# Kernel optimization log

Hardware: AMD Instinct MI355X
Metric: run time of the kernel (lower is better)

## Reference

```python
import jax, jax.numpy as jnp
import numpy as np

N_A, N_P = 50000, 100000          # author / paper node counts
E_W, E_C = 1600000, 3200000       # writes & written_by edges, cites edges
NEG_SLOPE = 0.2                   # DGL GATConv default leaky_relu slope
EPS = 1e-12                       # F.normalize eps


def _gat(h_src, h_dst, src, dst, W, al, ar, b, n_dst):
    """DGL GATConv: fc -> per-head additive attention -> edge softmax -> weighted sum + bias."""
    H, F = al.shape
    fs = (h_src @ W.T).reshape(-1, H, F)            # [Ns, H, F]
    fd = (h_dst @ W.T).reshape(-1, H, F)            # [Nd, H, F]
    el = (fs * al).sum(-1)                          # [Ns, H]
    er = (fd * ar).sum(-1)                          # [Nd, H]
    e = jax.nn.leaky_relu(el[src] + er[dst], NEG_SLOPE)      # [E, H]
    m = jax.lax.stop_gradient(jax.ops.segment_max(e, dst, num_segments=n_dst))
    ex = jnp.exp(e - m[dst])
    s = jax.ops.segment_sum(ex, dst, num_segments=n_dst)
    a = ex / s[dst]                                 # edge softmax per dst node, per head
    rst = jax.ops.segment_sum(fs[src] * a[:, :, None], dst, num_segments=n_dst)
    return rst + b.reshape(H, F)                    # [Nd, H, F]


def _l2norm(x):
    return x / jnp.maximum(jnp.linalg.norm(x, axis=1, keepdims=True), EPS)


def setup_inputs() -> dict:
    key = jax.random.key(0)
    ks = iter(jax.random.split(key, 64))
    def nrm(shape, scale=0.1):
        return jax.random.normal(next(ks), shape, dtype=jnp.float32) * scale
    inp = {
        'feat_author': jax.random.normal(next(ks), (N_A, 128), dtype=jnp.float32),
        'feat_paper':  jax.random.normal(next(ks), (N_P, 256), dtype=jnp.float32),
        'fm_W_author': nrm((64, 128)), 'fm_b_author': nrm((64,)),
        'fm_W_paper':  nrm((64, 256)), 'fm_b_paper':  nrm((64,)),
    }
    for e in ('writes', 'written_by', 'cites'):
        inp[f'g1_{e}_W'] = nrm((64, 64)); inp[f'g1_{e}_al'] = nrm((4, 16))
        inp[f'g1_{e}_ar'] = nrm((4, 16)); inp[f'g1_{e}_b'] = nrm((64,))
        inp[f'g2_{e}_W'] = nrm((64, 64)); inp[f'g2_{e}_al'] = nrm((1, 64))
        inp[f'g2_{e}_ar'] = nrm((1, 64)); inp[f'g2_{e}_b'] = nrm((64,))
    inp['w_src'] = jax.random.randint(next(ks), (E_W,), 0, N_A, dtype=jnp.int32)
    inp['w_dst'] = jax.random.randint(next(ks), (E_W,), 0, N_P, dtype=jnp.int32)
    inp['wb_src'] = jax.random.randint(next(ks), (E_W,), 0, N_P, dtype=jnp.int32)
    inp['wb_dst'] = jax.random.randint(next(ks), (E_W,), 0, N_A, dtype=jnp.int32)
    inp['c_src'] = jax.random.randint(next(ks), (E_C,), 0, N_P, dtype=jnp.int32)
    inp['c_dst'] = jax.random.randint(next(ks), (E_C,), 0, N_P, dtype=jnp.int32)
    return inp


def reference(feat_author, feat_paper, fm_W_author, fm_b_author, fm_W_paper, fm_b_paper,
              g1_writes_W, g1_writes_al, g1_writes_ar, g1_writes_b,
              g2_writes_W, g2_writes_al, g2_writes_ar, g2_writes_b,
              g1_written_by_W, g1_written_by_al, g1_written_by_ar, g1_written_by_b,
              g2_written_by_W, g2_written_by_al, g2_written_by_ar, g2_written_by_b,
              g1_cites_W, g1_cites_al, g1_cites_ar, g1_cites_b,
              g2_cites_W, g2_cites_al, g2_cites_ar, g2_cites_b,
              w_src, w_dst, wb_src, wb_dst, c_src, c_dst):
    # FeatureMappingLayer: per-ntype Linear -> relu, out_dim 64
    h_a = jax.nn.relu(feat_author @ fm_W_author.T + fm_b_author)
    h_p = jax.nn.relu(feat_paper @ fm_W_paper.T + fm_b_paper)
    # NodeAttentionLayer: per-etype GATConv(64 -> 16, 4 heads), flatten, sum over incoming etypes
    h1_p = (_gat(h_a, h_p, w_src, w_dst, g1_writes_W, g1_writes_al, g1_writes_ar, g1_writes_b, N_P)
            + _gat(h_p, h_p, c_src, c_dst, g1_cites_W, g1_cites_al, g1_cites_ar, g1_cites_b, N_P)
           ).reshape(N_P, 64)
    h1_a = _gat(h_p, h_a, wb_src, wb_dst, g1_written_by_W, g1_written_by_al, g1_written_by_ar,
                g1_written_by_b, N_A).reshape(N_A, 64)
    # gat2: per-etype GATConv(64 -> 64, 1 head) on h1[:, :64] (== h1), squeeze, sum
    h2_p = (_gat(h1_a, h1_p, w_src, w_dst, g2_writes_W, g2_writes_al, g2_writes_ar, g2_writes_b, N_P)
            + _gat(h1_p, h1_p, c_src, c_dst, g2_cites_W, g2_cites_al, g2_cites_ar, g2_cites_b, N_P)
           ).reshape(N_P, 64)
    h2_a = _gat(h1_p, h1_a, wb_src, wb_dst, g2_written_by_W, g2_written_by_al, g2_written_by_ar,
                g2_written_by_b, N_A).reshape(N_A, 64)
    # F.normalize(p=2, dim=1)
    return (_l2norm(h2_a), _l2norm(h2_p))
```

## Files before the change

### kernel.cpp

```cpp
#include <hip/hip_runtime.h>
#include <hip/hip_bf16.h>

#define N_A 50000
#define N_P 100000
#define E_W 1600000
#define E_C 3200000
#define HA (N_A*64)
#define HP (N_P*64)

typedef __attribute__((ext_vector_type(8))) short short8_t;
typedef __attribute__((ext_vector_type(4))) float f32x4;

__device__ __forceinline__ unsigned short f2b(float f)
{
    __hip_bfloat16 b = __float2bfloat16(f);
    return *reinterpret_cast<unsigned short*>(&b);
}

__global__ __launch_bounds__(256) void gemm_fm2(
        const float* __restrict__ X0, const float* __restrict__ W0,
        const float* __restrict__ b0, float* __restrict__ out0, int M0, int K0, int nb0,
        const float* __restrict__ X1, const float* __restrict__ W1,
        const float* __restrict__ b1, float* __restrict__ out1, int M1, int K1)
{
    __shared__ unsigned short Xs[128][72];
    __shared__ unsigned short Wsh[64][72];
    const float *X, *W, *bias; float* out; int M, K, row0;
    if ((int)blockIdx.x < nb0) {
        X = X0; W = W0; bias = b0; out = out0; M = M0; K = K0; row0 = blockIdx.x * 128;
    } else {
        X = X1; W = W1; bias = b1; out = out1; M = M1; K = K1;
        row0 = ((int)blockIdx.x - nb0) * 128;
    }
    int tid = threadIdx.x, lane = tid & 63, wv = tid >> 6;
    int m = lane & 15, kb = lane >> 4;

    f32x4 acc[2][4];
#pragma unroll
    for (int rb = 0; rb < 2; ++rb)
#pragma unroll
        for (int cb = 0; cb < 4; ++cb) acc[rb][cb] = (f32x4){0.f, 0.f, 0.f, 0.f};

    for (int k0 = 0; k0 < K; k0 += 64) {
        int rbase = (tid >> 4) * 8;
        int c4 = (tid & 15) * 4;
#pragma unroll
        for (int i = 0; i < 8; ++i) {
            int rg = row0 + rbase + i; if (rg >= M) rg = M - 1;
            float4 v = *reinterpret_cast<const float4*>(&X[(long)rg * K + k0 + c4]);
            Xs[rbase + i][c4 + 0] = f2b(v.x);
            Xs[rbase + i][c4 + 1] = f2b(v.y);
            Xs[rbase + i][c4 + 2] = f2b(v.z);
            Xs[rbase + i][c4 + 3] = f2b(v.w);
        }
        int wr = tid >> 2;
        int wc = (tid & 3) * 16;
#pragma unroll
        for (int q = 0; q < 4; ++q) {
            float4 v = *reinterpret_cast<const float4*>(&W[(long)wr * K + k0 + wc + q * 4]);
            Wsh[wr][wc + q * 4 + 0] = f2b(v.x);
            Wsh[wr][wc + q * 4 + 1] = f2b(v.y);
            Wsh[wr][wc + q * 4 + 2] = f2b(v.z);
            Wsh[wr][wc + q * 4 + 3] = f2b(v.w);
        }
        __syncthreads();
#pragma unroll
        for (int kc = 0; kc < 2; ++kc) {
            short8_t a0 = *reinterpret_cast<const short8_t*>(&Xs[wv * 32 + m][kc * 32 + kb * 8]);
            short8_t a1 = *reinterpret_cast<const short8_t*>(&Xs[wv * 32 + 16 + m][kc * 32 + kb * 8]);
#pragma unroll
            for (int cb = 0; cb < 4; ++cb) {
                short8_t b = *reinterpret_cast<const short8_t*>(&Wsh[cb * 16 + m][kc * 32 + kb * 8]);
                acc[0][cb] = __builtin_amdgcn_mfma_f32_16x16x32_bf16(a0, b, acc[0][cb], 0, 0, 0);
                acc[1][cb] = __builtin_amdgcn_mfma_f32_16x16x32_bf16(a1, b, acc[1][cb], 0, 0, 0);
            }
        }
        __syncthreads();
    }

#pragma unroll
    for (int rb = 0; rb < 2; ++rb)
#pragma unroll
    for (int j = 0; j < 4; ++j) {
        int r = row0 + wv * 32 + rb * 16 + (lane >> 4) * 4 + j;
        if (r < M) {
#pragma unroll
            for (int cb = 0; cb < 4; ++cb) {
                int c = cb * 16 + m;
                float v = acc[rb][cb][j] + bias[c];
                out[(long)r * 64 + c] = fmaxf(v, 0.f);
            }
        }
    }
}

__global__ __launch_bounds__(256) void proj3(
        const float* __restrict__ X0, const float* __restrict__ W0,
        unsigned short* __restrict__ o0, int M0, int nb0,
        const float* __restrict__ X1, const float* __restrict__ W1,
        unsigned short* __restrict__ o1, int M1, int nb1,
        const float* __restrict__ X2, const float* __restrict__ W2,
        unsigned short* __restrict__ o2, int M2)
{
    __shared__ unsigned short Xs[128][72];
    __shared__ unsigned short Wsh[64][72];
    const float *X, *W; unsigned short* out; int M, row0;
    if ((int)blockIdx.x < nb0) {
        X = X0; W = W0; out = o0; M = M0; row0 = blockIdx.x * 128;
    } else if ((int)blockIdx.x < nb0 + nb1) {
        X = X1; W = W1; out = o1; M = M1; row0 = ((int)blockIdx.x - nb0) * 128;
    } else {
        X = X2; W = W2; out = o2; M = M2; row0 = ((int)blockIdx.x - nb0 - nb1) * 128;
    }
    int tid = threadIdx.x, lane = tid & 63, wv = tid >> 6;
    int m = lane & 15, kb = lane >> 4;

    int rbase = (tid >> 4) * 8;
    int c4 = (tid & 15) * 4;
#pragma unroll
    for (int i = 0; i < 8; ++i) {
        int rg = row0 + rbase + i; if (rg >= M) rg = M - 1;
        float4 v = *reinterpret_cast<const float4*>(&X[(long)rg * 64 + c4]);
        Xs[rbase + i][c4 + 0] = f2b(v.x);
        Xs[rbase + i][c4 + 1] = f2b(v.y);
        Xs[rbase + i][c4 + 2] = f2b(v.z);
        Xs[rbase + i][c4 + 3] = f2b(v.w);
    }
    int wr = tid >> 2;
    int wc = (tid & 3) * 16;
#pragma unroll
    for (int q = 0; q < 4; ++q) {
        float4 v = *reinterpret_cast<const float4*>(&W[(long)wr * 64 + wc + q * 4]);
        Wsh[wr][wc + q * 4 + 0] = f2b(v.x);
        Wsh[wr][wc + q * 4 + 1] = f2b(v.y);
        Wsh[wr][wc + q * 4 + 2] = f2b(v.z);
        Wsh[wr][wc + q * 4 + 3] = f2b(v.w);
    }
    __syncthreads();

    f32x4 acc[2][4];
#pragma unroll
    for (int rb = 0; rb < 2; ++rb)
#pragma unroll
        for (int cb = 0; cb < 4; ++cb) acc[rb][cb] = (f32x4){0.f, 0.f, 0.f, 0.f};
#pragma unroll
    for (int kc = 0; kc < 2; ++kc) {
        short8_t a0 = *reinterpret_cast<const short8_t*>(&Xs[wv * 32 + m][kc * 32 + kb * 8]);
        short8_t a1 = *reinterpret_cast<const short8_t*>(&Xs[wv * 32 + 16 + m][kc * 32 + kb * 8]);
#pragma unroll
        for (int cb = 0; cb < 4; ++cb) {
            short8_t b = *reinterpret_cast<const short8_t*>(&Wsh[cb * 16 + m][kc * 32 + kb * 8]);
            acc[0][cb] = __builtin_amdgcn_mfma_f32_16x16x32_bf16(a0, b, acc[0][cb], 0, 0, 0);
            acc[1][cb] = __builtin_amdgcn_mfma_f32_16x16x32_bf16(a1, b, acc[1][cb], 0, 0, 0);
        }
    }
#pragma unroll
    for (int rb = 0; rb < 2; ++rb)
#pragma unroll
    for (int j = 0; j < 4; ++j) {
        int r = row0 + wv * 32 + rb * 16 + (lane >> 4) * 4 + j;
        if (r < M) {
#pragma unroll
            for (int cb = 0; cb < 4; ++cb)
                out[(long)r * 64 + cb * 16 + m] = f2b(acc[rb][cb][j]);
        }
    }
}

struct PA { const float* W; const float* a; float* o; int H; };
__global__ void prep_attn12(PA p0, PA p1, PA p2, PA p3, PA p4, PA p5,
                            PA p6, PA p7, PA p8, PA p9, PA p10, PA p11)
{
    PA p;
    switch (blockIdx.x) {
        case 0: p = p0; break;  case 1: p = p1; break;  case 2: p = p2; break;
        case 3: p = p3; break;  case 4: p = p4; break;  case 5: p = p5; break;
        case 6: p = p6; break;  case 7: p = p7; break;  case 8: p = p8; break;
        case 9: p = p9; break;  case 10: p = p10; break; default: p = p11; break;
    }
    int k = threadIdx.x;
    int F = 64 / p.H;
    for (int hh = 0; hh < p.H; ++hh) {
        float s = 0.f;
        for (int f = 0; f < F; ++f)
            s = fmaf(p.W[(hh * F + f) * 64 + k], p.a[hh * F + f], s);
        p.o[k * p.H + hh] = s;
    }
}

__global__ __launch_bounds__(256) void attnvec_mat(
        const float* __restrict__ hP, int NPn,
        const float* __restrict__ fP0, float* __restrict__ oP0,
        const float* __restrict__ fP1, float* __restrict__ oP1,
        const float* __restrict__ fP2, float* __restrict__ oP2,
        const float* __restrict__ fP3, float* __restrict__ oP3,
        const float* __restrict__ hA, int NAn,
        const float* __restrict__ fA0, float* __restrict__ oA0,
        const float* __restrict__ fA1, float* __restrict__ oA1,
        int H, int hb)
{
    __shared__ float hs[64 * 66];
    int tid = threadIdx.x;
    int slotsP = (H == 4) ? 16 : 4;
    int npbP = 256 / slotsP;
    int blocksP = (NPn + npbP - 1) / npbP;

    const float* hsrc; int node0, npb, slots, ncols, N;
    const float* fv0; const float* fv1; const float* fv2; const float* fv3;
    float* ov0; float* ov1; float* ov2; float* ov3;
    if ((int)blockIdx.x < blocksP) {
        hsrc = hP; N = NPn; slots = slotsP; npb = npbP;
        node0 = blockIdx.x * npb;
        ncols = 4 * H;
        fv0 = fP0; ov0 = oP0; fv1 = fP1; ov1 = oP1;
        fv2 = fP2; ov2 = oP2; fv3 = fP3; ov3 = oP3;
    } else {
        int b = (int)blockIdx.x - blocksP;
        hsrc = hA; N = NAn;
        slots = (H == 4) ? 8 : 4; npb = 256 / slots;
        node0 = b * npb;
        ncols = 2 * H;
        fv0 = fA0; ov0 = oA0; fv1 = fA1; ov1 = oA1;
        fv2 = fA0; ov2 = oA0; fv3 = fA1; ov3 = oA1;
    }

    for (int idx = tid; idx < npb * 64; idx += 256) {
        int row = idx >> 6, k = idx & 63;
        int g = node0 + row; if (g >= N) g = N - 1;
        hs[row * 66 + k] = hsrc[(long)g * 64 + k];
    }
    __syncthreads();

    int sshift = (slots == 16) ? 4 : (slots == 8) ? 3 : 2;
    int nl = tid >> sshift;
    int c = tid & (slots - 1);
    int node = node0 + nl;
    if (node >= N || c >= ncols || nl >= npb) return;
    int f = c >> hb;
    int hh = c & (H - 1);
    const float* fv = (f == 0) ? fv0 : (f == 1) ? fv1 : (f == 2) ? fv2 : fv3;
    float* ov = (f == 0) ? ov0 : (f == 1) ? ov1 : (f == 2) ? ov2 : ov3;

    float s = 0.f;
    const float* hrow = &hs[nl * 66];
#pragma unroll 8
    for (int k = 0; k < 64; ++k)
        s = fmaf(hrow[k], fv[k * H + hh], s);
    ov[(long)node * H + hh] = s;
}

__global__ void bucket_hist3(const int* __restrict__ d0, int E0, int* __restrict__ b0,
                             const int* __restrict__ d1, int E1, int* __restrict__ b1,
                             const int* __restrict__ d2, int E2, int* __restrict__ b2,
                             int shift, int blocksPer)
{
    int g = blockIdx.x / blocksPer, bb = blockIdx.x - g * blocksPer;
    const int* dst = g == 0 ? d0 : g == 1 ? d1 : d2;
    int E = g == 0 ? E0 : g == 1 ? E1 : E2;
    int* bcnt = g == 0 ? b0 : g == 1 ? b1 : b2;
    __shared__ int h[256];
    int tid = threadIdx.x;
    h[tid] = 0;
    __syncthreads();
    for (long i = (long)bb * 256 + tid; i < E; i += (long)blocksPer * 256)
        atomicAdd(&h[dst[i] >> shift], 1);
    __syncthreads();
    if (h[tid]) atomicAdd(&bcnt[tid], h[tid]);
}

__global__ void bucket_scan3(int* __restrict__ bcnt, int* __restrict__ bstart,
                             int* __restrict__ gcur,
                             int* __restrict__ o0, int Nn0, int Ee0,
                             int* __restrict__ o1, int Nn1, int Ee1,
                             int* __restrict__ o2, int Nn2, int Ee2)
{
    int g = blockIdx.x;
    int* bc = bcnt + g * 256;
    int* bs = bstart + g * 257;
    int* gc = gcur + g * 256;
    int* offs = g == 0 ? o0 : g == 1 ? o1 : o2;
    int N = g == 0 ? Nn0 : g == 1 ? Nn1 : Nn2;
    int E = g == 0 ? Ee0 : g == 1 ? Ee1 : Ee2;
    __shared__ int sc[256];
    int tid = threadIdx.x;
    int v = bc[tid];
    sc[tid] = v;
    __syncthreads();
    for (int off = 1; off < 256; off <<= 1) {
        int t = (tid >= off) ? sc[tid - off] : 0;
        __syncthreads();
        sc[tid] += t;
        __syncthreads();
    }
    int excl = sc[tid] - v;
    bs[tid] = excl;
    gc[tid] = excl;
    if (tid == 255) bs[256] = E;
    if (tid == 0) offs[N] = E;
}

#define EPT 8
__global__ __launch_bounds__(256) void part_kernel(const int* __restrict__ src,
        const int* __restrict__ dst, int* __restrict__ gcur,
        uint2* __restrict__ pairs, int E, int NB, int shift)
{
    __shared__ int hcnt[256];
    __shared__ int hbase[256];
    int tid = threadIdx.x;
    long base = (long)blockIdx.x * (256 * EPT);
    for (int i = tid; i < NB; i += 256) hcnt[i] = 0;
    __syncthreads();
    int b[EPT], r[EPT], s[EPT], d[EPT];
#pragma unroll
    for (int k = 0; k < EPT; ++k) {
        long idx = base + k * 256 + tid;
        if (idx < E) {
            s[k] = src[idx]; d[k] = dst[idx];
            b[k] = d[k] >> shift;
            r[k] = atomicAdd(&hcnt[b[k]], 1);
        } else b[k] = -1;
    }
    __syncthreads();
    for (int i = tid; i < NB; i += 256) {
        if (hcnt[i]) hbase[i] = atomicAdd(&gcur[i], hcnt[i]);
    }
    __syncthreads();
#pragma unroll
    for (int k = 0; k < EPT; ++k) {
        if (b[k] >= 0)
            pairs[hbase[b[k]] + r[k]] = make_uint2((unsigned)s[k], (unsigned)d[k]);
    }
}

__global__ __launch_bounds__(512) void csr_finalize(const uint2* __restrict__ pairs,
        const int* __restrict__ bstart, int* __restrict__ offs, int* __restrict__ csr,
        int N, int shift)
{
    __shared__ int cnt[512];
    __shared__ int sc[512];
    int tid = threadIdx.x;
    int b = blockIdx.x;
    int d0 = b << shift;
    int pS = bstart[b], pE = bstart[b + 1];
    cnt[tid] = 0;
    __syncthreads();
    for (int i = pS + tid; i < pE; i += 512)
        atomicAdd(&cnt[pairs[i].y - d0], 1);
    __syncthreads();
    int v = cnt[tid];
    sc[tid] = v;
    __syncthreads();
    for (int off = 1; off < 512; off <<= 1) {
        int t = (tid >= off) ? sc[tid - off] : 0;
        __syncthreads();
        sc[tid] += t;
        __syncthreads();
    }
    int excl = sc[tid] - v;
    if (d0 + tid < N) offs[d0 + tid] = pS + excl;
    cnt[tid] = excl;
    __syncthreads();
    for (int i = pS + tid; i < pE; i += 512) {
        uint2 u = pairs[i];
        int p = atomicAdd(&cnt[u.y - d0], 1);
        csr[pS + p] = (int)u.x;
    }
}

__device__ __forceinline__ void gat_graph(int d, const int* __restrict__ offs,
        const int* __restrict__ csr, const float* __restrict__ el,
        const float* __restrict__ er, const unsigned short* __restrict__ P,
        int hshift, int lane, float* o)
{
    int H = 1 << hshift;
    int off = offs[d];
    int n = offs[d + 1] - off;
    if (n == 0) return;
    int g8 = lane >> 3;
    int fo = (lane & 7) * 8;
    int hf = (hshift == 2) ? ((lane & 7) >> 1) : 0;
    int h = lane & (H - 1);
    float erd = er[d * H + h];
    int estep = 64 >> hshift;
    float acc[8];
#pragma unroll
    for (int q = 0; q < 8; ++q) acc[q] = 0.f;
    float ssum = 0.f;

    for (int base = 0; base < n; base += estep) {
        int i = base + (lane >> hshift);
        int sn = 0; float a = 0.f;
        if (i < n) {
            sn = csr[off + i];
            float v = el[sn * H + h] + erd;
            v = v > 0.f ? v : 0.2f * v;
            a = __expf(v);
            ssum += a;
        }
        int rounds = min(estep, n - base);
#pragma unroll 2
        for (int r = 0; r * 8 < rounds; ++r) {
            int sl = r * 8 + g8;
            int lsn = sl << hshift;
            int s2 = __shfl(sn, lsn, 64);
            float a2 = __shfl(a, lsn | hf, 64);
            uint4 u = *reinterpret_cast<const uint4*>(&P[(long)s2 * 64 + fo]);
            acc[0] = fmaf(__uint_as_float(u.x << 16), a2, acc[0]);
            acc[1] = fmaf(__uint_as_float(u.x & 0xffff0000u), a2, acc[1]);
            acc[2] = fmaf(__uint_as_float(u.y << 16), a2, acc[2]);
            acc[3] = fmaf(__uint_as_float(u.y & 0xffff0000u), a2, acc[3]);
            acc[4] = fmaf(__uint_as_float(u.z << 16), a2, acc[4]);
            acc[5] = fmaf(__uint_as_float(u.z & 0xffff0000u), a2, acc[5]);
            acc[6] = fmaf(__uint_as_float(u.w << 16), a2, acc[6]);
            acc[7] = fmaf(__uint_as_float(u.w & 0xffff0000u), a2, acc[7]);
        }
    }

    for (int oo = H; oo < 64; oo <<= 1) ssum += __shfl_xor(ssum, oo, 64);
    float rinv = 1.f / __shfl(ssum, hf, 64);
#pragma unroll
    for (int q = 0; q < 8; ++q) {
        acc[q] += __shfl_xor(acc[q], 8, 64);
        acc[q] += __shfl_xor(acc[q], 16, 64);
        acc[q] += __shfl_xor(acc[q], 32, 64);
        o[q] = fmaf(acc[q], rinv, o[q]);
    }
}

__global__ void gat_fused(
        int NPn, const int* __restrict__ w_offs, const int* __restrict__ w_csr,
        const float* __restrict__ el_w, const float* __restrict__ er_w,
        const unsigned short* __restrict__ Pw,
        const int* __restrict__ c_offs, const int* __restrict__ c_csr,
        const float* __restrict__ el_c, const float* __restrict__ er_c,
        const unsigned short* __restrict__ Pc,
        const float* __restrict__ bP0, const float* __restrict__ bP1,
        float* __restrict__ outP,
        int NAn, const int* __restrict__ wb_offs, const int* __restrict__ wb_csr,
        const float* __restrict__ el_wb, const float* __restrict__ er_wb,
        const unsigned short* __restrict__ Pwb,
        const float* __restrict__ bA0, float* __restrict__ outA,
        int hshift, int doNorm)
{
    int blocksP = (NPn + 3) >> 2;
    int lane = threadIdx.x & 63;
    int sub = threadIdx.x >> 6;
    int fo = (lane & 7) * 8;
    float o[8];
    float* dst;

    if ((int)blockIdx.x < blocksP) {
        int d = ((int)blockIdx.x << 2) | sub;
        if (d >= NPn) return;
#pragma unroll
        for (int q = 0; q < 8; ++q) o[q] = bP0[fo + q] + bP1[fo + q];
        gat_graph(d, w_offs, w_csr, el_w, er_w, Pw, hshift, lane, o);
        gat_graph(d, c_offs, c_csr, el_c, er_c, Pc, hshift, lane, o);
        dst = outP + (long)d * 64;
    } else {
        int d = (((int)blockIdx.x - blocksP) << 2) | sub;
        if (d >= NAn) return;
#pragma unroll
        for (int q = 0; q < 8; ++q) o[q] = bA0[fo + q];
        gat_graph(d, wb_offs, wb_csr, el_wb, er_wb, Pwb, hshift, lane, o);
        dst = outA + (long)d * 64;
    }

    if (doNorm) {
        float ss = 0.f;
#pragma unroll
        for (int q = 0; q < 8; ++q) ss = fmaf(o[q], o[q], ss);
        ss += __shfl_xor(ss, 1, 64);
        ss += __shfl_xor(ss, 2, 64);
        ss += __shfl_xor(ss, 4, 64);
        float sc = 1.f / fmaxf(sqrtf(ss), 1e-12f);
#pragma unroll
        for (int q = 0; q < 8; ++q) o[q] *= sc;
    }
    if (lane < 8) {
        float4 o0, o1;
        o0.x = o[0]; o0.y = o[1]; o0.z = o[2]; o0.w = o[3];
        o1.x = o[4]; o1.y = o[5]; o1.z = o[6]; o1.w = o[7];
        *reinterpret_cast<float4*>(dst + fo) = o0;
        *reinterpret_cast<float4*>(dst + fo + 4) = o1;
    }
}

extern "C" void kernel_launch(void* const* d_in, const int* in_sizes, int n_in,
                              void* d_out, int out_size, void* d_ws, size_t ws_size,
                              hipStream_t stream)
{
    const float* feat_a = (const float*)d_in[0];
    const float* feat_p = (const float*)d_in[1];
    const float* fmWa = (const float*)d_in[2];
    const float* fmba = (const float*)d_in[3];
    const float* fmWp = (const float*)d_in[4];
    const float* fmbp = (const float*)d_in[5];
    const float* g1w_W = (const float*)d_in[6];  const float* g1w_al = (const float*)d_in[7];
    const float* g1w_ar = (const float*)d_in[8]; const float* g1w_b = (const float*)d_in[9];
    const float* g2w_W = (const float*)d_in[10]; const float* g2w_al = (const float*)d_in[11];
    const float* g2w_ar = (const float*)d_in[12]; const float* g2w_b = (const float*)d_in[13];
    const float* g1wb_W = (const float*)d_in[14]; const float* g1wb_al = (const float*)d_in[15];
    const float* g1wb_ar = (const float*)d_in[16]; const float* g1wb_b = (const float*)d_in[17];
    const float* g2wb_W = (const float*)d_in[18]; const float* g2wb_al = (const float*)d_in[19];
    const float* g2wb_ar = (const float*)d_in[20]; const float* g2wb_b = (const float*)d_in[21];
    const float* g1c_W = (const float*)d_in[22]; const float* g1c_al = (const float*)d_in[23];
    const float* g1c_ar = (const float*)d_in[24]; const float* g1c_b = (const float*)d_in[25];
    const float* g2c_W = (const float*)d_in[26]; const float* g2c_al = (const float*)d_in[27];
    const float* g2c_ar = (const float*)d_in[28]; const float* g2c_b = (const float*)d_in[29];
    const int* w_src = (const int*)d_in[30];
    const int* w_dst = (const int*)d_in[31];
    const int* wb_src = (const int*)d_in[32];
    const int* wb_dst = (const int*)d_in[33];
    const int* c_src = (const int*)d_in[34];
    const int* c_dst = (const int*)d_in[35];

    float* ws = (float*)d_ws;
    size_t off = 0;
    auto alloc = [&](size_t n) { float* p = ws + off; off += n; return p; };
    float* h_a  = alloc(HA);
    float* h_p  = alloc(HP);
    float* h1_p = alloc(HP);
    float* h1_a = alloc(HA);
    unsigned short* Pw  = (unsigned short*)alloc(HA / 2 + 16);
    unsigned short* Pc  = (unsigned short*)alloc(HP / 2 + 16);
    unsigned short* Pwb = (unsigned short*)alloc(HP / 2 + 16);
    float* el_w  = alloc((size_t)N_A * 4);
    float* er_w  = alloc((size_t)N_P * 4);
    float* el_c  = alloc((size_t)N_P * 4);
    float* er_c  = alloc((size_t)N_P * 4);
    float* el_wb = alloc((size_t)N_P * 4);
    float* er_wb = alloc((size_t)N_A * 4);
    float* fold  = alloc(12 * 256);
    int* w_offs  = (int*)alloc(N_P + 1);
    int* c_offs  = (int*)alloc(N_P + 1);
    int* wb_offs = (int*)alloc(N_A + 1);
    int* bcnt3   = (int*)alloc(3 * 256);
    int* bstart3 = (int*)alloc(3 * 257);
    int* gcur3   = (int*)alloc(3 * 256);
    int* w_csr   = (int*)alloc(E_W);
    int* c_csr   = (int*)alloc(E_C);
    int* wb_csr  = (int*)alloc(E_W);
    off = (off + 1) & ~(size_t)1;
    uint2* pairs = (uint2*)alloc((size_t)E_C * 2);

    float* wal_w1 = fold + 0*256,  *war_w1 = fold + 1*256;
    float* wal_c1 = fold + 2*256,  *war_c1 = fold + 3*256;
    float* wal_b1 = fold + 4*256,  *war_b1 = fold + 5*256;
    float* wal_w2 = fold + 6*256,  *war_w2 = fold + 7*256;
    float* wal_c2 = fold + 8*256,  *war_c2 = fold + 9*256;
    float* wal_b2 = fold + 10*256, *war_b2 = fold + 11*256;

    const int SHIFT = 9;
    int NB_P = (N_P + 511) >> 9;
    int NB_A = (N_A + 511) >> 9;

    hipMemsetAsync(bcnt3, 0, 3 * 256 * sizeof(int), stream);
    bucket_hist3<<<3 * 256, 256, 0, stream>>>(w_dst, E_W, bcnt3,
                                              c_dst, E_C, bcnt3 + 256,
                                              wb_dst, E_W, bcnt3 + 512, SHIFT, 256);
    bucket_scan3<<<3, 256, 0, stream>>>(bcnt3, bstart3, gcur3,
                                        w_offs, N_P, E_W,
                                        c_offs, N_P, E_C,
                                        wb_offs, N_A, E_W);
    part_kernel<<<(E_W + 2047) / 2048, 256, 0, stream>>>(w_src, w_dst, gcur3, pairs, E_W, NB_P, SHIFT);
    csr_finalize<<<NB_P, 512, 0, stream>>>(pairs, bstart3, w_offs, w_csr, N_P, SHIFT);
    part_kernel<<<(E_C + 2047) / 2048, 256, 0, stream>>>(c_src, c_dst, gcur3 + 256, pairs, E_C, NB_P, SHIFT);
    csr_finalize<<<NB_P, 512, 0, stream>>>(pairs, bstart3 + 257, c_offs, c_csr, N_P, SHIFT);
    part_kernel<<<(E_W + 2047) / 2048, 256, 0, stream>>>(wb_src, wb_dst, gcur3 + 512, pairs, E_W, NB_A, SHIFT);
    csr_finalize<<<NB_A, 512, 0, stream>>>(pairs, bstart3 + 514, wb_offs, wb_csr, N_A, SHIFT);

    prep_attn12<<<12, 64, 0, stream>>>(
        PA{g1w_W,  g1w_al,  wal_w1, 4}, PA{g1w_W,  g1w_ar,  war_w1, 4},
        PA{g1c_W,  g1c_al,  wal_c1, 4}, PA{g1c_W,  g1c_ar,  war_c1, 4},
        PA{g1wb_W, g1wb_al, wal_b1, 4}, PA{g1wb_W, g1wb_ar, war_b1, 4},
        PA{g2w_W,  g2w_al,  wal_w2, 1}, PA{g2w_W,  g2w_ar,  war_w2, 1},
        PA{g2c_W,  g2c_al,  wal_c2, 1}, PA{g2c_W,  g2c_ar,  war_c2, 1},
        PA{g2wb_W, g2wb_al, wal_b2, 1}, PA{g2wb_W, g2wb_ar, war_b2, 1});

    {
        int nb0 = (N_A + 127) / 128;
        int nb1 = (N_P + 127) / 128;
        gemm_fm2<<<nb0 + nb1, 256, 0, stream>>>(feat_a, fmWa, fmba, h_a, N_A, 128, nb0,
                                                feat_p, fmWp, fmbp, h_p, N_P, 256);
    }

    int nbA = (N_A + 127) / 128, nbP = (N_P + 127) / 128;
    int gatGrid = (N_P + 3) / 4 + (N_A + 3) / 4;

    {
        int npbP = 16, npbA = 32;
        int grid = (N_P + npbP - 1) / npbP + (N_A + npbA - 1) / npbA;
        attnvec_mat<<<grid, 256, 0, stream>>>(
            h_p, N_P, wal_c1, el_c, war_c1, er_c, war_w1, er_w, wal_b1, el_wb,
            h_a, N_A, wal_w1, el_w, war_b1, er_wb, 4, 2);
    }
    proj3<<<nbA + 2 * nbP, 256, 0, stream>>>(h_a, g1w_W, Pw, N_A, nbA,
                                             h_p, g1c_W, Pc, N_P, nbP,
                                             h_p, g1wb_W, Pwb, N_P);
    gat_fused<<<gatGrid, 256, 0, stream>>>(
        N_P, w_offs, w_csr, el_w, er_w, Pw,
        c_offs, c_csr, el_c, er_c, Pc, g1w_b, g1c_b, h1_p,
        N_A, wb_offs, wb_csr, el_wb, er_wb, Pwb, g1wb_b, h1_a, 2, 0);

    {
        int npbP = 64, npbA = 64;
        int grid = (N_P + npbP - 1) / npbP + (N_A + npbA - 1) / npbA;
        attnvec_mat<<<grid, 256, 0, stream>>>(
            h1_p, N_P, wal_c2, el_c, war_c2, er_c, war_w2, er_w, wal_b2, el_wb,
            h1_a, N_A, wal_w2, el_w, war_b2, er_wb, 1, 0);
    }
    proj3<<<nbA + 2 * nbP, 256, 0, stream>>>(h1_a, g2w_W, Pw, N_A, nbA,
                                             h1_p, g2c_W, Pc, N_P, nbP,
                                             h1_p, g2wb_W, Pwb, N_P);
    float* out = (float*)d_out;
    gat_fused<<<gatGrid, 256, 0, stream>>>(
        N_P, w_offs, w_csr, el_w, er_w, Pw,
        c_offs, c_csr, el_c, er_c, Pc, g2w_b, g2c_b, out + HA,
        N_A, wb_offs, wb_csr, el_wb, er_wb, Pwb, g2wb_b, out, 0, 1);
}
```

Baseline: 785.6 us.

## Batch CSR build for all edge types and prefetch neighbor indices in GAT loop

The three per-edge-type partition and CSR-finalize launches are merged into one partition kernel and one finalize kernel, each dispatching on block index. Each edge type gets its own pairs buffer, aliased onto the not-yet-written node-feature workspace, so the three types can run concurrently instead of serialising through one shared buffer. The GAT aggregation loop also software-prefetches the next chunk's CSR source indices and el values, hiding gather latency behind the current chunk's feature accumulation. The cost is a few more registers in the hot loop and a dependence on the workspace aliasing being safe.

```diff
diff --git a/kernel.cpp b/kernel.cpp
--- a/kernel.cpp
+++ b/kernel.cpp
@@ -300,15 +300,30 @@
 }
 
 #define EPT 8
-__global__ __launch_bounds__(256) void part_kernel(const int* __restrict__ src,
-        const int* __restrict__ dst, int* __restrict__ gcur,
-        uint2* __restrict__ pairs, int E, int NB, int shift)
-{
+__global__ __launch_bounds__(256) void part3(
+        const int* __restrict__ s0, const int* __restrict__ d0, int E0, int nb0,
+        uint2* __restrict__ p0,
+        const int* __restrict__ s1, const int* __restrict__ d1, int E1, int nb1,
+        uint2* __restrict__ p1,
+        const int* __restrict__ s2g, const int* __restrict__ d2g, int E2,
+        uint2* __restrict__ p2,
+        int* __restrict__ gcur3, int shift)
+{
+    const int* src; const int* dst; int E; uint2* pairs; int* gcur; long base;
+    if ((int)blockIdx.x < nb0) {
+        src = s0; dst = d0; E = E0; pairs = p0; gcur = gcur3;
+        base = (long)blockIdx.x * (256 * EPT);
+    } else if ((int)blockIdx.x < nb0 + nb1) {
+        src = s1; dst = d1; E = E1; pairs = p1; gcur = gcur3 + 256;
+        base = (long)((int)blockIdx.x - nb0) * (256 * EPT);
+    } else {
+        src = s2g; dst = d2g; E = E2; pairs = p2; gcur = gcur3 + 512;
+        base = (long)((int)blockIdx.x - nb0 - nb1) * (256 * EPT);
+    }
     __shared__ int hcnt[256];
     __shared__ int hbase[256];
     int tid = threadIdx.x;
-    long base = (long)blockIdx.x * (256 * EPT);
-    for (int i = tid; i < NB; i += 256) hcnt[i] = 0;
+    hcnt[tid] = 0;
     __syncthreads();
     int b[EPT], r[EPT], s[EPT], d[EPT];
 #pragma unroll
@@ -321,9 +336,7 @@
         } else b[k] = -1;
     }
     __syncthreads();
-    for (int i = tid; i < NB; i += 256) {
-        if (hcnt[i]) hbase[i] = atomicAdd(&gcur[i], hcnt[i]);
-    }
+    if (hcnt[tid]) hbase[tid] = atomicAdd(&gcur[tid], hcnt[tid]);
     __syncthreads();
 #pragma unroll
     for (int k = 0; k < EPT; ++k) {
@@ -332,14 +345,27 @@
     }
 }
 
-__global__ __launch_bounds__(512) void csr_finalize(const uint2* __restrict__ pairs,
-        const int* __restrict__ bstart, int* __restrict__ offs, int* __restrict__ csr,
-        int N, int shift)
-{
+__global__ __launch_bounds__(512) void csr_fin3(
+        const uint2* __restrict__ p0, const int* __restrict__ bs0,
+        int* __restrict__ of0, int* __restrict__ c0, int N0, int NB0,
+        const uint2* __restrict__ p1, const int* __restrict__ bs1,
+        int* __restrict__ of1, int* __restrict__ c1, int N1, int NB1,
+        const uint2* __restrict__ p2, const int* __restrict__ bs2,
+        int* __restrict__ of2, int* __restrict__ c2, int N2,
+        int shift)
+{
+    const uint2* pairs; const int* bstart; int* offs; int* csr; int N, b;
+    if ((int)blockIdx.x < NB0) {
+        pairs = p0; bstart = bs0; offs = of0; csr = c0; N = N0; b = blockIdx.x;
+    } else if ((int)blockIdx.x < NB0 + NB1) {
+        pairs = p1; bstart = bs1; offs = of1; csr = c1; N = N1; b = (int)blockIdx.x - NB0;
+    } else {
+        pairs = p2; bstart = bs2; offs = of2; csr = c2; N = N2;
+        b = (int)blockIdx.x - NB0 - NB1;
+    }
     __shared__ int cnt[512];
     __shared__ int sc[512];
     int tid = threadIdx.x;
-    int b = blockIdx.x;
     int d0 = b << shift;
     int pS = bstart[b], pE = bstart[b + 1];
     cnt[tid] = 0;
@@ -382,17 +408,23 @@
     int h = lane & (H - 1);
     float erd = er[d * H + h];
     int estep = 64 >> hshift;
+    int i0 = lane >> hshift;
     float acc[8];
 #pragma unroll
     for (int q = 0; q < 8; ++q) acc[q] = 0.f;
     float ssum = 0.f;
 
+    int sn_c = 0; float elv_c = 0.f;
+    if (i0 < n) { sn_c = csr[off + i0]; elv_c = el[sn_c * H + h]; }
+
     for (int base = 0; base < n; base += estep) {
-        int i = base + (lane >> hshift);
-        int sn = 0; float a = 0.f;
-        if (i < n) {
-            sn = csr[off + i];
-            float v = el[sn * H + h] + erd;
+        int inext = base + estep + i0;
+        int sn_n = 0; float elv_n = 0.f;
+        if (inext < n) { sn_n = csr[off + inext]; elv_n = el[sn_n * H + h]; }
+
+        float a = 0.f;
+        if (base + i0 < n) {
+            float v = elv_c + erd;
             v = v > 0.f ? v : 0.2f * v;
             a = __expf(v);
             ssum += a;
@@ -402,7 +434,7 @@
         for (int r = 0; r * 8 < rounds; ++r) {
             int sl = r * 8 + g8;
             int lsn = sl << hshift;
-            int s2 = __shfl(sn, lsn, 64);
+            int s2 = __shfl(sn_c, lsn, 64);
             float a2 = __shfl(a, lsn | hf, 64);
             uint4 u = *reinterpret_cast<const uint4*>(&P[(long)s2 * 64 + fo]);
             acc[0] = fmaf(__uint_as_float(u.x << 16), a2, acc[0]);
@@ -414,6 +446,7 @@
             acc[6] = fmaf(__uint_as_float(u.w << 16), a2, acc[6]);
             acc[7] = fmaf(__uint_as_float(u.w & 0xffff0000u), a2, acc[7]);
         }
+        sn_c = sn_n; elv_c = elv_n;
     }
 
     for (int oo = H; oo < 64; oo <<= 1) ssum += __shfl_xor(ssum, oo, 64);
@@ -522,6 +555,9 @@
     float* h_p  = alloc(HP);
     float* h1_p = alloc(HP);
     float* h1_a = alloc(HA);
+    uint2* pairs_w  = (uint2*)h_a;
+    uint2* pairs_c  = (uint2*)h_a + E_W;
+    uint2* pairs_wb = (uint2*)h_a + E_W + E_C;
     unsigned short* Pw  = (unsigned short*)alloc(HA / 2 + 16);
     unsigned short* Pc  = (unsigned short*)alloc(HP / 2 + 16);
     unsigned short* Pwb = (unsigned short*)alloc(HP / 2 + 16);
@@ -541,8 +577,6 @@
     int* w_csr   = (int*)alloc(E_W);
     int* c_csr   = (int*)alloc(E_C);
     int* wb_csr  = (int*)alloc(E_W);
-    off = (off + 1) & ~(size_t)1;
-    uint2* pairs = (uint2*)alloc((size_t)E_C * 2);
 
     float* wal_w1 = fold + 0*256,  *war_w1 = fold + 1*256;
     float* wal_c1 = fold + 2*256,  *war_c1 = fold + 3*256;
@@ -563,12 +597,17 @@
                                         w_offs, N_P, E_W,
                                         c_offs, N_P, E_C,
                                         wb_offs, N_A, E_W);
-    part_kernel<<<(E_W + 2047) / 2048, 256, 0, stream>>>(w_src, w_dst, gcur3, pairs, E_W, NB_P, SHIFT);
-    csr_finalize<<<NB_P, 512, 0, stream>>>(pairs, bstart3, w_offs, w_csr, N_P, SHIFT);
-    part_kernel<<<(E_C + 2047) / 2048, 256, 0, stream>>>(c_src, c_dst, gcur3 + 256, pairs, E_C, NB_P, SHIFT);
-    csr_finalize<<<NB_P, 512, 0, stream>>>(pairs, bstart3 + 257, c_offs, c_csr, N_P, SHIFT);
-    part_kernel<<<(E_W + 2047) / 2048, 256, 0, stream>>>(wb_src, wb_dst, gcur3 + 512, pairs, E_W, NB_A, SHIFT);
-    csr_finalize<<<NB_A, 512, 0, stream>>>(pairs, bstart3 + 514, wb_offs, wb_csr, N_A, SHIFT);
+    {
+        int nbW = (E_W + 2047) / 2048, nbC = (E_C + 2047) / 2048;
+        part3<<<nbW + nbC + nbW, 256, 0, stream>>>(
+            w_src, w_dst, E_W, nbW, pairs_w,
+            c_src, c_dst, E_C, nbC, pairs_c,
+            wb_src, wb_dst, E_W, pairs_wb, gcur3, SHIFT);
+        csr_fin3<<<NB_P + NB_P + NB_A, 512, 0, stream>>>(
+            pairs_w, bstart3, w_offs, w_csr, N_P, NB_P,
+            pairs_c, bstart3 + 257, c_offs, c_csr, N_P, NB_P,
+            pairs_wb, bstart3 + 514, wb_offs, wb_csr, N_A, SHIFT);
+    }
 
     prep_attn12<<<12, 64, 0, stream>>>(
         PA{g1w_W,  g1w_al,  wal_w1, 4}, PA{g1w_W,  g1w_ar,  war_w1, 4},
```

After: 735.4 us. 1.07x faster.
